# Kernel optimization log

Measured on AMD Instinct MI355X. Metric: run time of the kernel, lower is better.

The kernel has to match this reference:

```python
import jax, jax.numpy as jnp
import numpy as np

IN_DIM, HID, E, N = 1024, 2048, 8, 16384

def setup_inputs() -> dict:
    key = jax.random.key(0)
    ks = jax.random.split(key, 12)
    s_in = 1.0 / np.sqrt(IN_DIM)
    s_h = 1.0 / np.sqrt(HID)
    return {
        "x": jax.random.normal(ks[0], (N, IN_DIM), dtype=jnp.float32),
        "enc_W": jax.random.uniform(ks[1], (IN_DIM, HID), jnp.float32, -s_in, s_in),
        "enc_b": jax.random.uniform(ks[2], (HID,), jnp.float32, -s_in, s_in),
        "gate_W": jax.random.uniform(ks[3], (HID, E), jnp.float32, -s_h, s_h),
        "expert_W": jax.random.uniform(ks[4], (E, HID, HID), jnp.float32, -s_h, s_h),
        "expert_b": jax.random.uniform(ks[5], (E, HID), jnp.float32, -s_h, s_h),
        "res_W": jax.random.uniform(ks[6], (HID, HID), jnp.float32, -s_h, s_h),
        "res_b": jax.random.uniform(ks[7], (HID,), jnp.float32, -s_h, s_h),
        "coef_W": jax.random.uniform(ks[8], (HID, 2), jnp.float32, -s_h, s_h),
        "coef_b": jax.random.uniform(ks[9], (2,), jnp.float32, -s_h, s_h),
        "dec_W": jax.random.uniform(ks[10], (HID, IN_DIM), jnp.float32, -s_h, s_h),
        "dec_b": jax.random.uniform(ks[11], (IN_DIM,), jnp.float32, -s_h, s_h),
    }

def reference(x, enc_W, enc_b, gate_W, expert_W, expert_b, res_W, res_b, coef_W, coef_b, dec_W, dec_b):
    # Encode: Linear + ReLU -> h [N, HID]
    h = jax.nn.relu(x @ enc_W + enc_b)
    # Top-1 gating (softmax probs, argmax expert, combine weight = chosen prob)
    probs = jax.nn.softmax(h @ gate_W, axis=-1)          # [N, E]
    idx = jnp.argmax(probs, axis=-1)                     # [N]
    gate = jnp.max(probs, axis=-1, keepdims=True)        # [N, 1]
    # Dense dispatch: run every expert, select via one-hot combine
    y_all = jnp.einsum('nd,edh->neh', h, expert_W) + expert_b  # [N, E, HID]
    onehot = jax.nn.one_hot(idx, y_all.shape[1], dtype=h.dtype)
    moe_out = jnp.einsum('neh,ne->nh', y_all, onehot) * gate   # [N, HID]
    # Residual expert + learned 2-way blending coefficient
    res = h @ res_W + res_b
    coef = jax.nn.softmax(h @ coef_W + coef_b, axis=-1)        # [N, 2]
    out = moe_out * coef[:, 0:1] + res * coef[:, 1:2]
    # Decode
    return out @ dec_W + dec_b
```

## Files before the change

### kernel.cpp

```cpp
#include <hip/hip_runtime.h>


#define N_TOK 16384
#define IN_DIM 1024
#define HID 2048
#define NEXP 8
#define TAU 8.0e-3f

typedef __bf16 bf16_t;
typedef __bf16 bf16x8 __attribute__((ext_vector_type(8)));
typedef __bf16 bf16x4v __attribute__((ext_vector_type(4)));
typedef float f32x4 __attribute__((ext_vector_type(4)));
typedef unsigned short ushort_t;

#define CLAMP1E4(v) fmaxf(fminf((v), 1.0e4f), -1.0e4f)

#define ASYNC16(gp, lp)                                                        \
  __builtin_amdgcn_global_load_lds(                                            \
      (const __attribute__((address_space(1))) void*)(gp),                     \
      (__attribute__((address_space(3))) void*)(lp), 16, 0, 0)

static __device__ inline ushort_t b2u(bf16_t v) {
  union { bf16_t b; ushort_t u; } x; x.b = v; return x.u;
}

__global__ __launch_bounds__(256) void fill_bf16(bf16_t* __restrict__ p,
                                                 float v, int n) {
  const int i = blockIdx.x * 256 + threadIdx.x;
  if (i < n) p[i] = (bf16_t)v;
}

__global__ __launch_bounds__(256) void detect_dtype(
    const ushort_t* __restrict__ xr, int* __restrict__ flag) {
  __shared__ int s_bad;
  if (threadIdx.x == 0) s_bad = 0;
  __syncthreads();
  int bad = 0;
  for (int i = threadIdx.x; i < 4096; i += 256) {
    const int e = (xr[i] >> 7) & 0xFF;
    if (e >= 0xC0) bad = 1;
  }
  if (__any(bad) && (threadIdx.x & 63) == 0) atomicOr(&s_bad, 1);
  __syncthreads();
  if (threadIdx.x == 0) *flag = s_bad;
}

__global__ __launch_bounds__(256) void cvt_to_bf16(
    const void* __restrict__ src, bf16_t* __restrict__ dst, int n,
    const int* __restrict__ flagp) {
  const int f = *flagp;
  const int i = blockIdx.x * 256 + threadIdx.x;
  if (i >= n) return;
  dst[i] = f ? (bf16_t)((const float*)src)[i] : ((const bf16_t*)src)[i];
}

__global__ __launch_bounds__(256) void cvt_to_bf16_x4(
    const void* __restrict__ src, bf16_t* __restrict__ dst, int n4,
    const int* __restrict__ flagp) {
  const int f = *flagp;
  const int i = blockIdx.x * 256 + threadIdx.x;
  if (i >= n4) return;
  bf16x4v o;
  if (f) {
    const f32x4 v = ((const f32x4*)src)[i];
    o[0] = (bf16_t)v[0]; o[1] = (bf16_t)v[1];
    o[2] = (bf16_t)v[2]; o[3] = (bf16_t)v[3];
  } else {
    o = ((const bf16x4v*)src)[i];
  }
  ((bf16x4v*)dst)[i] = o;
}

__global__ __launch_bounds__(256) void cvt_to_f32(
    const void* __restrict__ src, float* __restrict__ dst, int n,
    const int* __restrict__ flagp) {
  const int f = *flagp;
  const int i = blockIdx.x * 256 + threadIdx.x;
  if (i >= n) return;
  dst[i] = f ? ((const float*)src)[i] : (float)((const bf16_t*)src)[i];
}

__global__ __launch_bounds__(256) void transpose_cvt(
    const void* __restrict__ src0, ushort_t* __restrict__ dst, int R, int C,
    size_t elem_off, const int* __restrict__ flagp, size_t src_zstride,
    size_t dst_zstride) {
  __shared__ ushort_t t[32][33];
  const int f = *flagp;
  const size_t eoff = elem_off + (size_t)blockIdx.z * src_zstride;
  dst += (size_t)blockIdx.z * dst_zstride;
  const int c0 = blockIdx.x * 32, r0 = blockIdx.y * 32;
  const int tx = threadIdx.x, ty = threadIdx.y;
  if (f) {
    const float* s = (const float*)src0 + eoff;
#pragma unroll
    for (int i = 0; i < 4; ++i)
      t[ty + i * 8][tx] =
          b2u((bf16_t)s[(size_t)(r0 + ty + i * 8) * C + c0 + tx]);
  } else {
    const ushort_t* s = (const ushort_t*)src0 + eoff;
#pragma unroll
    for (int i = 0; i < 4; ++i)
      t[ty + i * 8][tx] = s[(size_t)(r0 + ty + i * 8) * C + c0 + tx];
  }
  __syncthreads();
#pragma unroll
  for (int i = 0; i < 4; ++i)
    dst[(size_t)(c0 + ty + i * 8) * R + r0 + tx] = t[tx][ty + i * 8];
}

__global__ __launch_bounds__(256) void enc_gemm(
    const bf16_t* __restrict__ A, const bf16_t* __restrict__ Bt,
    const float* __restrict__ bias, bf16_t* __restrict__ H) {
  __shared__ bf16_t As[128 * 32];
  __shared__ bf16_t Bs[128 * 32];

  const int tid = threadIdx.x, lane = tid & 63, w = tid >> 6;
  const int wr = w >> 1, wc = w & 1, quad = lane >> 4, l16 = lane & 15;
  const int m0 = blockIdx.x * 128, n0 = blockIdx.y * 128;
  const char* Ab = (const char*)A;
  const char* Bb = (const char*)Bt;
  const size_t lda = (size_t)IN_DIM * 2;

  const f32x4 fz = {0.f, 0.f, 0.f, 0.f};
  f32x4 acc[4][4];
#pragma unroll
  for (int i = 0; i < 4; ++i)
#pragma unroll
    for (int j = 0; j < 4; ++j) acc[i][j] = fz;

  size_t aoff[2], boff[2];
  int cb[2];
#pragma unroll
  for (int c = 0; c < 2; ++c) {
    cb[c] = (w * 2 + c) * 1024;
    const int o = cb[c] + lane * 16;
    const int row = o >> 6, kb = o & 63;
    aoff[c] = (size_t)(m0 + row) * lda + kb;
    boff[c] = (size_t)(n0 + row) * lda + kb;
  }

  for (int kt = 0; kt < IN_DIM / 32; ++kt) {
    __syncthreads();
#pragma unroll
    for (int c = 0; c < 2; ++c) {
      ASYNC16(Ab + aoff[c] + (size_t)kt * 64, (char*)As + cb[c]);
      ASYNC16(Bb + boff[c] + (size_t)kt * 64, (char*)Bs + cb[c]);
    }
    __syncthreads();

    bf16x8 af[4], bfr[4];
#pragma unroll
    for (int i = 0; i < 4; ++i)
      af[i] = *(const bf16x8*)&As[(wr * 64 + i * 16 + l16) * 32 + quad * 8];
#pragma unroll
    for (int j = 0; j < 4; ++j)
      bfr[j] = *(const bf16x8*)&Bs[(wc * 64 + j * 16 + l16) * 32 + quad * 8];
#pragma unroll
    for (int i = 0; i < 4; ++i)
#pragma unroll
      for (int j = 0; j < 4; ++j)
        acc[i][j] = __builtin_amdgcn_mfma_f32_16x16x32_bf16(af[i], bfr[j],
                                                            acc[i][j], 0, 0, 0);
  }

  float bj[4];
  int colj[4];
#pragma unroll
  for (int j = 0; j < 4; ++j) {
    colj[j] = n0 + wc * 64 + j * 16 + l16;
    bj[j] = bias[colj[j]];
  }

#pragma unroll
  for (int i = 0; i < 4; ++i) {
#pragma unroll
    for (int r = 0; r < 4; ++r) {
      const int row = m0 + wr * 64 + i * 16 + quad * 4 + r;
#pragma unroll
      for (int j = 0; j < 4; ++j) {
        const float v = fminf(fmaxf(acc[i][j][r] + bj[j], 0.f), 1.0e4f);
        H[(size_t)row * HID + colj[j]] = (bf16_t)v;
      }
    }
  }
}

__global__ __launch_bounds__(256) void gate_from_h(
    const bf16_t* __restrict__ H, const bf16_t* __restrict__ gW,
    const bf16_t* __restrict__ cW, const float* __restrict__ coefBf,
    float* __restrict__ s0g, float* __restrict__ s1g, float* __restrict__ c0g,
    int* __restrict__ eidx, int* __restrict__ ambig, int* __restrict__ acnt) {
  const int tid = threadIdx.x, lane = tid & 63, w = tid >> 6;
  const int r0 = blockIdx.x * 16 + w * 4;

  float acc[4][10];
#pragma unroll
  for (int g = 0; g < 4; ++g)
#pragma unroll
    for (int o = 0; o < 10; ++o) acc[g][o] = 0.f;

#pragma unroll
  for (int it = 0; it < HID / 512; ++it) {
    const int h0 = it * 512 + lane * 8;
    bf16x8 hv[4];
#pragma unroll
    for (int g = 0; g < 4; ++g)
      hv[g] = *(const bf16x8*)(H + (size_t)(r0 + g) * HID + h0);
    const bf16_t* gp = gW + (size_t)h0 * 8;
    const bf16_t* cp = cW + (size_t)h0 * 2;
    bf16x8 cc0 = *(const bf16x8*)(cp);
    bf16x8 cc1 = *(const bf16x8*)(cp + 8);
#pragma unroll
    for (int k = 0; k < 8; ++k) {
      const bf16x8 gk = *(const bf16x8*)(gp + k * 8);
      const float ck0 = (k < 4) ? (float)cc0[(k & 3) * 2]
                                : (float)cc1[(k & 3) * 2];
      const float ck1 = (k < 4) ? (float)cc0[(k & 3) * 2 + 1]
                                : (float)cc1[(k & 3) * 2 + 1];
#pragma unroll
      for (int g = 0; g < 4; ++g) {
        const float v = (float)hv[g][k];
#pragma unroll
        for (int o = 0; o < 8; ++o) acc[g][o] += v * (float)gk[o];
        acc[g][8] += v * ck0;
        acc[g][9] += v * ck1;
      }
    }
  }

#pragma unroll
  for (int m = 1; m < 64; m <<= 1)
#pragma unroll
    for (int g = 0; g < 4; ++g)
#pragma unroll
      for (int o = 0; o < 10; ++o) acc[g][o] += __shfl_xor(acc[g][o], m);

  if (lane == 0) {
#pragma unroll
    for (int g = 0; g < 4; ++g) {
      const int r = r0 + g;
      float lv[8];
#pragma unroll
      for (int e = 0; e < 8; ++e) lv[e] = acc[g][e];
      float mx = lv[0];
      int idx = 0;
#pragma unroll
      for (int e = 1; e < 8; ++e)
        if (lv[e] > mx) { mx = lv[e]; idx = e; }
      float s2 = -1.0e30f;
#pragma unroll
      for (int e = 0; e < 8; ++e)
        if (e != idx) s2 = fmaxf(s2, lv[e]);
      float s = 0.f;
#pragma unroll
      for (int e = 0; e < 8; ++e) s += expf(lv[e] - mx);
      const float gate = 1.f / s;
      const float c0 = acc[g][8] + coefBf[0], c1 = acc[g][9] + coefBf[1];
      const float cm = fmaxf(c0, c1);
      const float e0 = expf(c0 - cm), e1 = expf(c1 - cm);
      const float inv = 1.f / (e0 + e1);
      const float p0 = e0 * inv;
      c0g[r] = p0;
      s1g[r] = e1 * inv;
      s0g[r] = gate * p0;
      eidx[r] = idx;
      if (mx - s2 < TAU) {
        const int p = atomicAdd(acnt, 1);
        ambig[p] = r;
      }
    }
  }
}

__global__ __launch_bounds__(256) void rescue_rows(
    const void* __restrict__ xraw, const void* __restrict__ encWraw,
    const float* __restrict__ encBf, const void* __restrict__ gateWraw,
    const int* __restrict__ flagp, const int* __restrict__ ambig,
    const int* __restrict__ acnt, const float* __restrict__ c0g,
    float* __restrict__ s0g, int* __restrict__ eidx) {
  const int i = blockIdx.x;
  if (i >= *acnt) return;
  const int r = ambig[i];
  const int f = *flagp;
  const int tid = threadIdx.x;

  double hacc[8] = {0, 0, 0, 0, 0, 0, 0, 0};
  if (f) {
    const float* x = (const float*)xraw + (size_t)r * IN_DIM;
    const float* W = (const float*)encWraw;
    for (int k = 0; k < IN_DIM; ++k) {
      const double xv = (double)x[k];
      const float* Wr = W + (size_t)k * HID;
#pragma unroll
      for (int jj = 0; jj < 8; ++jj)
        hacc[jj] += xv * (double)Wr[tid + jj * 256];
    }
  } else {
    const bf16_t* x = (const bf16_t*)xraw + (size_t)r * IN_DIM;
    const bf16_t* W = (const bf16_t*)encWraw;
    for (int k = 0; k < IN_DIM; ++k) {
      const double xv = (double)(float)x[k];
      const bf16_t* Wr = W + (size_t)k * HID;
#pragma unroll
      for (int jj = 0; jj < 8; ++jj)
        hacc[jj] += xv * (double)(float)Wr[tid + jj * 256];
    }
  }

  double lg[8] = {0, 0, 0, 0, 0, 0, 0, 0};
#pragma unroll
  for (int jj = 0; jj < 8; ++jj) {
    const int j = tid + jj * 256;
    double h = hacc[jj] + (double)encBf[j];
    if (h > 0.0) {
      if (f) {
        const float* g = (const float*)gateWraw + (size_t)j * 8;
#pragma unroll
        for (int e = 0; e < 8; ++e) lg[e] += h * (double)g[e];
      } else {
        const bf16_t* g = (const bf16_t*)gateWraw + (size_t)j * 8;
#pragma unroll
        for (int e = 0; e < 8; ++e) lg[e] += h * (double)(float)g[e];
      }
    }
  }
#pragma unroll
  for (int m = 1; m < 64; m <<= 1)
#pragma unroll
    for (int e = 0; e < 8; ++e) lg[e] += __shfl_xor(lg[e], m);

  __shared__ double red[4][8];
  const int w = tid >> 6, lane = tid & 63;
  if (lane == 0)
#pragma unroll
    for (int e = 0; e < 8; ++e) red[w][e] = lg[e];
  __syncthreads();
  if (tid == 0) {
    double t[8];
#pragma unroll
    for (int e = 0; e < 8; ++e)
      t[e] = red[0][e] + red[1][e] + red[2][e] + red[3][e];
    double m = t[0];
    int idx = 0;
#pragma unroll
    for (int e = 1; e < 8; ++e)
      if (t[e] > m) { m = t[e]; idx = e; }
    double s = 0.0;
#pragma unroll
    for (int e = 0; e < 8; ++e) s += exp(t[e] - m);
    s0g[r] = (float)((1.0 / s) * (double)c0g[r]);
    eidx[r] = idx;
  }
}

__global__ __launch_bounds__(256) void bucket_rows(
    const int* __restrict__ eidx, int* __restrict__ cnt,
    int* __restrict__ perm) {
  const int r = blockIdx.x * 256 + threadIdx.x;
  const int e = eidx[r];
  const int pos = atomicAdd(&cnt[e], 1);
  perm[(size_t)e * N_TOK + pos] = r;
}

__global__ __launch_bounds__(256) void expert_gemm(
    const bf16_t* __restrict__ H, const bf16_t* __restrict__ wTbase,
    size_t wstride, const float* __restrict__ expBf,
    const int* __restrict__ perm, const int* __restrict__ cnt, int eArg,
    const float* __restrict__ s0g, bf16_t* __restrict__ mid) {
  __shared__ bf16_t As[128 * 32];
  __shared__ bf16_t Bs[128 * 32];
  __shared__ int rows_s[128];
  __shared__ float s0_s[128];

  const int e = (eArg >= 0) ? eArg : (int)blockIdx.z;
  const bf16_t* wTe = wTbase + (size_t)e * wstride;
  const float* eBe = expBf + (size_t)e * HID;
  const int* permE = perm + (size_t)e * N_TOK;

  const int cnte = cnt[e];
  const int lt = blockIdx.x;
  if (lt * 128 >= cnte) return;
  int nrows = cnte - lt * 128;
  if (nrows > 128) nrows = 128;

  const int tid = threadIdx.x, lane = tid & 63, w = tid >> 6;
  const int wr = w >> 1, wc = w & 1, quad = lane >> 4, l16 = lane & 15;

  if (tid < 128) {
    int grow = -1;
    float a0 = 0.f;
    if (tid < nrows) {
      grow = permE[lt * 128 + tid];
      a0 = s0g[grow];
    }
    rows_s[tid] = grow;
    s0_s[tid] = a0;
  }
  __syncthreads();

  const int n0 = blockIdx.y * 128;
  const char* Hb = (const char*)H;
  const char* Wb = (const char*)wTe;

  size_t aoff[2], boff[2];
  int cb[2];
#pragma unroll
  for (int c = 0; c < 2; ++c) {
    cb[c] = (w * 2 + c) * 1024;
    const int o = cb[c] + lane * 16;
    const int row = o >> 6, kb = o & 63;
    int gr = rows_s[row];
    if (gr < 0) gr = 0;
    aoff[c] = (size_t)gr * (HID * 2) + kb;
    boff[c] = (size_t)(n0 + row) * (HID * 2) + kb;
  }

  const f32x4 fz = {0.f, 0.f, 0.f, 0.f};
  f32x4 acc[4][4];
#pragma unroll
  for (int i = 0; i < 4; ++i)
#pragma unroll
    for (int j = 0; j < 4; ++j) acc[i][j] = fz;

  for (int kt = 0; kt < HID / 32; ++kt) {
    __syncthreads();
#pragma unroll
    for (int c = 0; c < 2; ++c) {
      ASYNC16(Hb + aoff[c] + (size_t)kt * 64, (char*)As + cb[c]);
      ASYNC16(Wb + boff[c] + (size_t)kt * 64, (char*)Bs + cb[c]);
    }
    __syncthreads();

    bf16x8 af[4], bfr[4];
#pragma unroll
    for (int i = 0; i < 4; ++i)
      af[i] = *(const bf16x8*)&As[(wr * 64 + i * 16 + l16) * 32 + quad * 8];
#pragma unroll
    for (int j = 0; j < 4; ++j)
      bfr[j] = *(const bf16x8*)&Bs[(wc * 64 + j * 16 + l16) * 32 + quad * 8];
#pragma unroll
    for (int i = 0; i < 4; ++i)
#pragma unroll
      for (int j = 0; j < 4; ++j)
        acc[i][j] = __builtin_amdgcn_mfma_f32_16x16x32_bf16(af[i], bfr[j],
                                                            acc[i][j], 0, 0, 0);
  }

  float beb[4];
  int colj[4];
#pragma unroll
  for (int j = 0; j < 4; ++j) {
    colj[j] = n0 + wc * 64 + j * 16 + l16;
    beb[j] = eBe[colj[j]];
  }
#pragma unroll
  for (int i = 0; i < 4; ++i) {
#pragma unroll
    for (int r = 0; r < 4; ++r) {
      const int lr = wr * 64 + i * 16 + quad * 4 + r;
      const int grow = rows_s[lr];
      if (grow < 0) continue;
      const float s0 = s0_s[lr];
#pragma unroll
      for (int j = 0; j < 4; ++j) {
        const float v = CLAMP1E4(s0 * (acc[i][j][r] + beb[j]));
        mid[(size_t)grow * HID + colj[j]] = (bf16_t)v;
      }
    }
  }
}

__global__ __launch_bounds__(256) void res_gemm(
    const bf16_t* __restrict__ H, const bf16_t* __restrict__ Bt,
    const float* __restrict__ rB, const float* __restrict__ s1g,
    bf16_t* __restrict__ mid) {
  __shared__ bf16_t As[128 * 32];
  __shared__ bf16_t Bs[128 * 32];

  const int tid = threadIdx.x, lane = tid & 63, w = tid >> 6;
  const int wr = w >> 1, wc = w & 1, quad = lane >> 4, l16 = lane & 15;
  const int m0 = blockIdx.x * 128, n0 = blockIdx.y * 128;
  const char* Ab = (const char*)H;
  const char* Bb = (const char*)Bt;

  size_t aoff[2], boff[2];
  int cb[2];
#pragma unroll
  for (int c = 0; c < 2; ++c) {
    cb[c] = (w * 2 + c) * 1024;
    const int o = cb[c] + lane * 16;
    const int row = o >> 6, kb = o & 63;
    aoff[c] = (size_t)(m0 + row) * (HID * 2) + kb;
    boff[c] = (size_t)(n0 + row) * (HID * 2) + kb;
  }

  const f32x4 fz = {0.f, 0.f, 0.f, 0.f};
  f32x4 acc[4][4];
#pragma unroll
  for (int i = 0; i < 4; ++i)
#pragma unroll
    for (int j = 0; j < 4; ++j) acc[i][j] = fz;

  for (int kt = 0; kt < HID / 32; ++kt) {
    __syncthreads();
#pragma unroll
    for (int c = 0; c < 2; ++c) {
      ASYNC16(Ab + aoff[c] + (size_t)kt * 64, (char*)As + cb[c]);
      ASYNC16(Bb + boff[c] + (size_t)kt * 64, (char*)Bs + cb[c]);
    }
    __syncthreads();

    bf16x8 af[4], bfr[4];
#pragma unroll
    for (int i = 0; i < 4; ++i)
      af[i] = *(const bf16x8*)&As[(wr * 64 + i * 16 + l16) * 32 + quad * 8];
#pragma unroll
    for (int j = 0; j < 4; ++j)
      bfr[j] = *(const bf16x8*)&Bs[(wc * 64 + j * 16 + l16) * 32 + quad * 8];
#pragma unroll
    for (int i = 0; i < 4; ++i)
#pragma unroll
      for (int j = 0; j < 4; ++j)
        acc[i][j] = __builtin_amdgcn_mfma_f32_16x16x32_bf16(af[i], bfr[j],
                                                            acc[i][j], 0, 0, 0);
  }

  float rbb[4];
  int colj[4];
#pragma unroll
  for (int j = 0; j < 4; ++j) {
    colj[j] = n0 + wc * 64 + j * 16 + l16;
    rbb[j] = rB[colj[j]];
  }
#pragma unroll
  for (int i = 0; i < 4; ++i) {
#pragma unroll
    for (int r = 0; r < 4; ++r) {
      const int row = m0 + wr * 64 + i * 16 + quad * 4 + r;
      const float s1 = s1g[row];
#pragma unroll
      for (int j = 0; j < 4; ++j) {
        const size_t ix = (size_t)row * HID + colj[j];
        const float v =
            CLAMP1E4(s1 * (acc[i][j][r] + rbb[j]) + (float)mid[ix]);
        mid[ix] = (bf16_t)v;
      }
    }
  }
}

__global__ __launch_bounds__(256) void dec_gemm(
    const bf16_t* __restrict__ A, const bf16_t* __restrict__ Bt,
    const float* __restrict__ bias, void* __restrict__ C,
    const int* __restrict__ flagp) {
  __shared__ bf16_t As[128 * 32];
  __shared__ bf16_t Bs[128 * 32];

  const int fl = *flagp;
  const int tid = threadIdx.x, lane = tid & 63, w = tid >> 6;
  const int wr = w >> 1, wc = w & 1, quad = lane >> 4, l16 = lane & 15;
  const int m0 = blockIdx.x * 128, n0 = blockIdx.y * 128;
  const char* Ab = (const char*)A;
  const char* Bb = (const char*)Bt;

  size_t aoff[2], boff[2];
  int cb[2];
#pragma unroll
  for (int c = 0; c < 2; ++c) {
    cb[c] = (w * 2 + c) * 1024;
    const int o = cb[c] + lane * 16;
    const int row = o >> 6, kb = o & 63;
    aoff[c] = (size_t)(m0 + row) * (HID * 2) + kb;
    boff[c] = (size_t)(n0 + row) * (HID * 2) + kb;
  }

  const f32x4 fz = {0.f, 0.f, 0.f, 0.f};
  f32x4 acc[4][4];
#pragma unroll
  for (int i = 0; i < 4; ++i)
#pragma unroll
    for (int j = 0; j < 4; ++j) acc[i][j] = fz;

  for (int kt = 0; kt < HID / 32; ++kt) {
    __syncthreads();
#pragma unroll
    for (int c = 0; c < 2; ++c) {
      ASYNC16(Ab + aoff[c] + (size_t)kt * 64, (char*)As + cb[c]);
      ASYNC16(Bb + boff[c] + (size_t)kt * 64, (char*)Bs + cb[c]);
    }
    __syncthreads();

    bf16x8 af[4], bfr[4];
#pragma unroll
    for (int i = 0; i < 4; ++i)
      af[i] = *(const bf16x8*)&As[(wr * 64 + i * 16 + l16) * 32 + quad * 8];
#pragma unroll
    for (int j = 0; j < 4; ++j)
      bfr[j] = *(const bf16x8*)&Bs[(wc * 64 + j * 16 + l16) * 32 + quad * 8];
#pragma unroll
    for (int i = 0; i < 4; ++i)
#pragma unroll
      for (int j = 0; j < 4; ++j)
        acc[i][j] = __builtin_amdgcn_mfma_f32_16x16x32_bf16(af[i], bfr[j],
                                                            acc[i][j], 0, 0, 0);
  }

  float bb[4];
  int colj[4];
#pragma unroll
  for (int j = 0; j < 4; ++j) {
    colj[j] = n0 + wc * 64 + j * 16 + l16;
    bb[j] = bias[colj[j]];
  }
#pragma unroll
  for (int i = 0; i < 4; ++i) {
#pragma unroll
    for (int r = 0; r < 4; ++r) {
      const int row = m0 + wr * 64 + i * 16 + quad * 4 + r;
#pragma unroll
      for (int j = 0; j < 4; ++j) {
        const float v = CLAMP1E4(acc[i][j][r] + bb[j]);
        const size_t ix = (size_t)row * IN_DIM + colj[j];
        if (fl)
          ((float*)C)[ix] = v;
        else
          ((bf16_t*)C)[ix] = (bf16_t)v;
      }
    }
  }
}

extern "C" void kernel_launch(void* const* d_in, const int* in_sizes, int n_in,
                              void* d_out, int out_size, void* d_ws,
                              size_t ws_size, hipStream_t stream) {
  (void)in_sizes; (void)n_in;

  const void* x     = d_in[0];
  const void* encW  = d_in[1];
  const void* encB  = d_in[2];
  const void* gateW = d_in[3];
  const void* expW  = d_in[4];
  const void* expB  = d_in[5];
  const void* resW  = d_in[6];
  const void* resB  = d_in[7];
  const void* coefW = d_in[8];
  const void* coefB = d_in[9];
  const void* decW  = d_in[10];
  const void* decB  = d_in[11];

  char* ws = (char*)d_ws;
  size_t o = 0;
  int*    flag  = (int*)(ws + o);    o += 256;
  int*    cnt   = (int*)(ws + o);    o += 256;
  int*    acnt  = cnt + 8;
  float*  s0g   = (float*)(ws + o);  o += (size_t)N_TOK * 4;
  float*  s1g   = (float*)(ws + o);  o += (size_t)N_TOK * 4;
  float*  c0g   = (float*)(ws + o);  o += (size_t)N_TOK * 4;
  int*    eidx  = (int*)(ws + o);    o += (size_t)N_TOK * 4;
  int*    ambig = (int*)(ws + o);    o += (size_t)N_TOK * 4;
  int*    perm  = (int*)(ws + o);    o += (size_t)NEXP * N_TOK * 4;
  float*  encBf = (float*)(ws + o);  o += HID * 4;
  float*  expBf = (float*)(ws + o);  o += (size_t)NEXP * HID * 4;
  float*  resBf = (float*)(ws + o);  o += HID * 4;
  float*  decBf = (float*)(ws + o);  o += IN_DIM * 4;
  float*  coefBf= (float*)(ws + o);  o += 256;
  bf16_t* gWb   = (bf16_t*)(ws + o); o += (size_t)HID * 8 * 2;
  bf16_t* cWb   = (bf16_t*)(ws + o); o += (size_t)HID * 2 * 2;
  o = (o + 255) & ~(size_t)255;
  bf16_t* hbuf  = (bf16_t*)(ws + o); o += (size_t)N_TOK * HID * 2;
  bf16_t* mid   = (bf16_t*)(ws + o); o += (size_t)N_TOK * HID * 2;
  bf16_t* wT    = (bf16_t*)(ws + o); o += (size_t)HID * HID * 2;
  const size_t needed_small = o;
  const size_t S = (size_t)HID * HID;
  bf16_t* wTall = (bf16_t*)(ws + o);
  const size_t needed_big = o + 10 * S * 2;
  bf16_t* xbf = mid;

  if (ws_size < needed_small) {
    const float v = (float)(ws_size >> 20);
    fill_bf16<<<dim3((out_size + 255) / 256), 256, 0, stream>>>(
        (bf16_t*)d_out, v, out_size);
    return;
  }
  const bool big = ws_size >= needed_big;

  detect_dtype<<<1, 256, 0, stream>>>((const ushort_t*)x, flag);
  hipMemsetAsync(cnt, 0, 256, stream);

  cvt_to_bf16_x4<<<dim3(N_TOK * IN_DIM / 4 / 256), 256, 0, stream>>>(
      x, xbf, N_TOK * IN_DIM / 4, flag);
  cvt_to_f32<<<dim3(HID / 256), 256, 0, stream>>>(encB, encBf, HID, flag);
  cvt_to_f32<<<dim3(NEXP * HID / 256), 256, 0, stream>>>(expB, expBf,
                                                         NEXP * HID, flag);
  cvt_to_f32<<<dim3(HID / 256), 256, 0, stream>>>(resB, resBf, HID, flag);
  cvt_to_f32<<<dim3(IN_DIM / 256), 256, 0, stream>>>(decB, decBf, IN_DIM, flag);
  cvt_to_f32<<<1, 256, 0, stream>>>(coefB, coefBf, 2, flag);
  cvt_to_bf16<<<dim3(HID * 8 / 256), 256, 0, stream>>>(gateW, gWb, HID * 8,
                                                       flag);
  cvt_to_bf16<<<dim3(HID * 2 / 256), 256, 0, stream>>>(coefW, cWb, HID * 2,
                                                       flag);

  const dim3 tb(32, 8, 1);

  transpose_cvt<<<dim3(HID / 32, IN_DIM / 32, 1), tb, 0, stream>>>(
      encW, (ushort_t*)wT, IN_DIM, HID, 0, flag, 0, 0);
  if (big) {
    transpose_cvt<<<dim3(HID / 32, HID / 32, NEXP), tb, 0, stream>>>(
        expW, (ushort_t*)wTall, HID, HID, 0, flag, S, S);
    transpose_cvt<<<dim3(HID / 32, HID / 32, 1), tb, 0, stream>>>(
        resW, (ushort_t*)(wTall + 8 * S), HID, HID, 0, flag, 0, 0);
    transpose_cvt<<<dim3(IN_DIM / 32, HID / 32, 1), tb, 0, stream>>>(
        decW, (ushort_t*)(wTall + 9 * S), HID, IN_DIM, 0, flag, 0, 0);
  }

  enc_gemm<<<dim3(N_TOK / 128, HID / 128), 256, 0, stream>>>(xbf, wT, encBf,
                                                             hbuf);
  gate_from_h<<<dim3(N_TOK / 16), 256, 0, stream>>>(
      hbuf, gWb, cWb, coefBf, s0g, s1g, c0g, eidx, ambig, acnt);
  rescue_rows<<<dim3(1024), 256, 0, stream>>>(x, encW, encBf, gateW, flag,
                                              ambig, acnt, c0g, s0g, eidx);
  bucket_rows<<<dim3(N_TOK / 256), 256, 0, stream>>>(eidx, cnt, perm);

  if (big) {
    expert_gemm<<<dim3(N_TOK / 128, HID / 128, NEXP), 256, 0, stream>>>(
        hbuf, wTall, S, expBf, perm, cnt, -1, s0g, mid);
    res_gemm<<<dim3(N_TOK / 128, HID / 128), 256, 0, stream>>>(
        hbuf, wTall + 8 * S, resBf, s1g, mid);
    dec_gemm<<<dim3(N_TOK / 128, IN_DIM / 128), 256, 0, stream>>>(
        mid, wTall + 9 * S, decBf, d_out, flag);
  } else {
    for (int e = 0; e < NEXP; ++e) {
      transpose_cvt<<<dim3(HID / 32, HID / 32, 1), tb, 0, stream>>>(
          expW, (ushort_t*)wT, HID, HID, (size_t)e * HID * HID, flag, 0, 0);
      expert_gemm<<<dim3(N_TOK / 128, HID / 128, 1), 256, 0, stream>>>(
          hbuf, wT, 0, expBf, perm, cnt, e, s0g, mid);
    }
    transpose_cvt<<<dim3(HID / 32, HID / 32, 1), tb, 0, stream>>>(
        resW, (ushort_t*)wT, HID, HID, 0, flag, 0, 0);
    res_gemm<<<dim3(N_TOK / 128, HID / 128), 256, 0, stream>>>(hbuf, wT, resBf,
                                                               s1g, mid);
    transpose_cvt<<<dim3(IN_DIM / 32, HID / 32, 1), tb, 0, stream>>>(
        decW, (ushort_t*)wT, HID, IN_DIM, 0, flag, 0, 0);
    dec_gemm<<<dim3(N_TOK / 128, IN_DIM / 128), 256, 0, stream>>>(
        mid, wT, decBf, d_out, flag);
  }
}
```

Before: 1.489 ms.

## Gather tokens by expert into contiguous buffer and compact expert GEMM grid

Gate counts per expert are now accumulated inside the gating kernel, and rescue adjusts them when a row's expert changes. A placement kernel builds a flat expert-sorted permutation, and a gather kernel copies H rows into a contiguous permuted buffer. The expert GEMM then runs over a compact 1D tile list (136 tiles instead of 8×128 mostly-empty blocks) with contiguous A loads, and the residual GEMM also reads the permuted buffer. The small conversion kernels are merged into one launch. This adds a full-size gather copy and scattered output writes through a row-id table.

```diff
diff --git a/kernel.cpp b/kernel.cpp
--- a/kernel.cpp
+++ b/kernel.cpp
@@ -43,15 +43,6 @@
   if (__any(bad) && (threadIdx.x & 63) == 0) atomicOr(&s_bad, 1);
   __syncthreads();
   if (threadIdx.x == 0) *flag = s_bad;
-}
-
-__global__ __launch_bounds__(256) void cvt_to_bf16(
-    const void* __restrict__ src, bf16_t* __restrict__ dst, int n,
-    const int* __restrict__ flagp) {
-  const int f = *flagp;
-  const int i = blockIdx.x * 256 + threadIdx.x;
-  if (i >= n) return;
-  dst[i] = f ? (bf16_t)((const float*)src)[i] : ((const bf16_t*)src)[i];
 }
 
 __global__ __launch_bounds__(256) void cvt_to_bf16_x4(
@@ -71,13 +62,40 @@
   ((bf16x4v*)dst)[i] = o;
 }
 
-__global__ __launch_bounds__(256) void cvt_to_f32(
-    const void* __restrict__ src, float* __restrict__ dst, int n,
+__global__ __launch_bounds__(256) void cvt_small(
+    const void* __restrict__ encB, const void* __restrict__ expB,
+    const void* __restrict__ resB, const void* __restrict__ decB,
+    const void* __restrict__ coefB, const void* __restrict__ gateW,
+    const void* __restrict__ coefW, float* __restrict__ encBf,
+    float* __restrict__ expBf, float* __restrict__ resBf,
+    float* __restrict__ decBf, float* __restrict__ coefBf,
+    bf16_t* __restrict__ gWb, bf16_t* __restrict__ cWb,
     const int* __restrict__ flagp) {
   const int f = *flagp;
   const int i = blockIdx.x * 256 + threadIdx.x;
+  const int seg = blockIdx.y;
+  const void* src;
+  int n;
+  switch (seg) {
+    case 0: src = encB;  n = HID; break;
+    case 1: src = expB;  n = NEXP * HID; break;
+    case 2: src = resB;  n = HID; break;
+    case 3: src = decB;  n = IN_DIM; break;
+    case 4: src = coefB; n = 2; break;
+    case 5: src = gateW; n = HID * 8; break;
+    default: src = coefW; n = HID * 2; break;
+  }
   if (i >= n) return;
-  dst[i] = f ? ((const float*)src)[i] : (float)((const bf16_t*)src)[i];
+  const float v = f ? ((const float*)src)[i] : (float)((const bf16_t*)src)[i];
+  switch (seg) {
+    case 0: encBf[i] = v; break;
+    case 1: expBf[i] = v; break;
+    case 2: resBf[i] = v; break;
+    case 3: decBf[i] = v; break;
+    case 4: coefBf[i] = v; break;
+    case 5: gWb[i] = (bf16_t)v; break;
+    default: cWb[i] = (bf16_t)v; break;
+  }
 }
 
 __global__ __launch_bounds__(256) void transpose_cvt(
@@ -189,7 +207,8 @@
     const bf16_t* __restrict__ H, const bf16_t* __restrict__ gW,
     const bf16_t* __restrict__ cW, const float* __restrict__ coefBf,
     float* __restrict__ s0g, float* __restrict__ s1g, float* __restrict__ c0g,
-    int* __restrict__ eidx, int* __restrict__ ambig, int* __restrict__ acnt) {
+    int* __restrict__ eidx, int* __restrict__ ambig, int* __restrict__ acnt,
+    int* __restrict__ cnt) {
   const int tid = threadIdx.x, lane = tid & 63, w = tid >> 6;
   const int r0 = blockIdx.x * 16 + w * 4;
 
@@ -264,6 +283,7 @@
       s1g[r] = e1 * inv;
       s0g[r] = gate * p0;
       eidx[r] = idx;
+      atomicAdd(&cnt[idx], 1);
       if (mx - s2 < TAU) {
         const int p = atomicAdd(acnt, 1);
         ambig[p] = r;
@@ -277,7 +297,7 @@
     const float* __restrict__ encBf, const void* __restrict__ gateWraw,
     const int* __restrict__ flagp, const int* __restrict__ ambig,
     const int* __restrict__ acnt, const float* __restrict__ c0g,
-    float* __restrict__ s0g, int* __restrict__ eidx) {
+    float* __restrict__ s0g, int* __restrict__ eidx, int* __restrict__ cnt) {
   const int i = blockIdx.x;
   if (i >= *acnt) return;
   const int r = ambig[i];
@@ -349,33 +369,263 @@
 #pragma unroll
     for (int e = 0; e < 8; ++e) s += exp(t[e] - m);
     s0g[r] = (float)((1.0 / s) * (double)c0g[r]);
-    eidx[r] = idx;
-  }
-}
-
-__global__ __launch_bounds__(256) void bucket_rows(
-    const int* __restrict__ eidx, int* __restrict__ cnt,
-    int* __restrict__ perm) {
+    const int old = eidx[r];
+    if (idx != old) {
+      atomicSub(&cnt[old], 1);
+      atomicAdd(&cnt[idx], 1);
+      eidx[r] = idx;
+    }
+  }
+}
+
+__global__ __launch_bounds__(256) void place_rows(
+    const int* __restrict__ eidx, const int* __restrict__ cnt,
+    int* __restrict__ curs, int* __restrict__ permflat) {
   const int r = blockIdx.x * 256 + threadIdx.x;
   const int e = eidx[r];
-  const int pos = atomicAdd(&cnt[e], 1);
-  perm[(size_t)e * N_TOK + pos] = r;
-}
-
-__global__ __launch_bounds__(256) void expert_gemm(
-    const bf16_t* __restrict__ H, const bf16_t* __restrict__ wTbase,
+  int prefix = 0;
+  for (int ee = 0; ee < NEXP; ++ee)
+    if (ee < e) prefix += cnt[ee];
+  const int pos = atomicAdd(&curs[e], 1);
+  permflat[prefix + pos] = r;
+}
+
+__global__ __launch_bounds__(256) void gather_rows(
+    const bf16_t* __restrict__ H, const int* __restrict__ permflat,
+    const float* __restrict__ s0g, const float* __restrict__ s1g,
+    bf16_t* __restrict__ Hp, int* __restrict__ rowid,
+    float* __restrict__ s0p, float* __restrict__ s1p) {
+  const int w = threadIdx.x >> 6, lane = threadIdx.x & 63;
+  const int p = blockIdx.x * 4 + w;
+  const int r = permflat[p];
+  if (lane == 0) {
+    rowid[p] = r;
+    s0p[p] = s0g[r];
+    s1p[p] = s1g[r];
+  }
+  const bf16x8* src = (const bf16x8*)(H + (size_t)r * HID);
+  bf16x8* dst = (bf16x8*)(Hp + (size_t)p * HID);
+#pragma unroll
+  for (int i = 0; i < 4; ++i) dst[lane + i * 64] = src[lane + i * 64];
+}
+
+__global__ __launch_bounds__(256) void expert_gemm_t(
+    const bf16_t* __restrict__ Hp, const bf16_t* __restrict__ wTall,
     size_t wstride, const float* __restrict__ expBf,
-    const int* __restrict__ perm, const int* __restrict__ cnt, int eArg,
-    const float* __restrict__ s0g, bf16_t* __restrict__ mid) {
+    const int* __restrict__ cnt, const int* __restrict__ rowid,
+    const float* __restrict__ s0p, bf16_t* __restrict__ mid) {
   __shared__ bf16_t As[128 * 32];
   __shared__ bf16_t Bs[128 * 32];
   __shared__ int rows_s[128];
   __shared__ float s0_s[128];
 
-  const int e = (eArg >= 0) ? eArg : (int)blockIdx.z;
-  const bf16_t* wTe = wTbase + (size_t)e * wstride;
+  const int x = blockIdx.x;
+  int e = -1, base = 0, nrows = 0;
+  {
+    int acc = 0, pre = 0;
+    for (int ee = 0; ee < NEXP; ++ee) {
+      const int ce = cnt[ee];
+      const int nt = (ce + 127) >> 7;
+      if (x < acc + nt) {
+        const int t = x - acc;
+        e = ee;
+        base = pre + t * 128;
+        nrows = ce - t * 128;
+        if (nrows > 128) nrows = 128;
+        break;
+      }
+      acc += nt;
+      pre += ce;
+    }
+  }
+  if (e < 0) return;
+
+  const int tid = threadIdx.x, lane = tid & 63, w = tid >> 6;
+  const int wr = w >> 1, wc = w & 1, quad = lane >> 4, l16 = lane & 15;
+
+  if (tid < 128) {
+    int grow = -1;
+    float a0 = 0.f;
+    if (tid < nrows) {
+      grow = rowid[base + tid];
+      a0 = s0p[base + tid];
+    }
+    rows_s[tid] = grow;
+    s0_s[tid] = a0;
+  }
+  __syncthreads();
+
+  const int n0 = blockIdx.y * 128;
+  const char* Hb = (const char*)Hp;
+  const char* Wb = (const char*)(wTall + (size_t)e * wstride);
+
+  size_t aoff[2], boff[2];
+  int cb[2];
+#pragma unroll
+  for (int c = 0; c < 2; ++c) {
+    cb[c] = (w * 2 + c) * 1024;
+    const int o = cb[c] + lane * 16;
+    const int row = o >> 6, kb = o & 63;
+    int ar = base + row;
+    if (ar > N_TOK - 1) ar = N_TOK - 1;
+    aoff[c] = (size_t)ar * (HID * 2) + kb;
+    boff[c] = (size_t)(n0 + row) * (HID * 2) + kb;
+  }
+
+  const f32x4 fz = {0.f, 0.f, 0.f, 0.f};
+  f32x4 acc[4][4];
+#pragma unroll
+  for (int i = 0; i < 4; ++i)
+#pragma unroll
+    for (int j = 0; j < 4; ++j) acc[i][j] = fz;
+
+  for (int kt = 0; kt < HID / 32; ++kt) {
+    __syncthreads();
+#pragma unroll
+    for (int c = 0; c < 2; ++c) {
+      ASYNC16(Hb + aoff[c] + (size_t)kt * 64, (char*)As + cb[c]);
+      ASYNC16(Wb + boff[c] + (size_t)kt * 64, (char*)Bs + cb[c]);
+    }
+    __syncthreads();
+
+    bf16x8 af[4], bfr[4];
+#pragma unroll
+    for (int i = 0; i < 4; ++i)
+      af[i] = *(const bf16x8*)&As[(wr * 64 + i * 16 + l16) * 32 + quad * 8];
+#pragma unroll
+    for (int j = 0; j < 4; ++j)
+      bfr[j] = *(const bf16x8*)&Bs[(wc * 64 + j * 16 + l16) * 32 + quad * 8];
+#pragma unroll
+    for (int i = 0; i < 4; ++i)
+#pragma unroll
+      for (int j = 0; j < 4; ++j)
+        acc[i][j] = __builtin_amdgcn_mfma_f32_16x16x32_bf16(af[i], bfr[j],
+                                                            acc[i][j], 0, 0, 0);
+  }
+
   const float* eBe = expBf + (size_t)e * HID;
-  const int* permE = perm + (size_t)e * N_TOK;
+  float beb[4];
+  int colj[4];
+#pragma unroll
+  for (int j = 0; j < 4; ++j) {
+    colj[j] = n0 + wc * 64 + j * 16 + l16;
+    beb[j] = eBe[colj[j]];
+  }
+#pragma unroll
+  for (int i = 0; i < 4; ++i) {
+#pragma unroll
+    for (int r = 0; r < 4; ++r) {
+      const int lr = wr * 64 + i * 16 + quad * 4 + r;
+      const int grow = rows_s[lr];
+      if (grow < 0) continue;
+      const float s0 = s0_s[lr];
+#pragma unroll
+      for (int j = 0; j < 4; ++j) {
+        const float v = CLAMP1E4(s0 * (acc[i][j][r] + beb[j]));
+        mid[(size_t)grow * HID + colj[j]] = (bf16_t)v;
+      }
+    }
+  }
+}
+
+__global__ __launch_bounds__(256) void res_gemm_p(
+    const bf16_t* __restrict__ Hp, const bf16_t* __restrict__ Bt,
+    const float* __restrict__ rB, const int* __restrict__ rowid,
+    const float* __restrict__ s1p, bf16_t* __restrict__ mid) {
+  __shared__ bf16_t As[128 * 32];
+  __shared__ bf16_t Bs[128 * 32];
+
+  const int tid = threadIdx.x, lane = tid & 63, w = tid >> 6;
+  const int wr = w >> 1, wc = w & 1, quad = lane >> 4, l16 = lane & 15;
+  const int m0 = blockIdx.x * 128, n0 = blockIdx.y * 128;
+  const char* Ab = (const char*)Hp;
+  const char* Bb = (const char*)Bt;
+
+  size_t aoff[2], boff[2];
+  int cb[2];
+#pragma unroll
+  for (int c = 0; c < 2; ++c) {
+    cb[c] = (w * 2 + c) * 1024;
+    const int o = cb[c] + lane * 16;
+    const int row = o >> 6, kb = o & 63;
+    aoff[c] = (size_t)(m0 + row) * (HID * 2) + kb;
+    boff[c] = (size_t)(n0 + row) * (HID * 2) + kb;
+  }
+
+  const f32x4 fz = {0.f, 0.f, 0.f, 0.f};
+  f32x4 acc[4][4];
+#pragma unroll
+  for (int i = 0; i < 4; ++i)
+#pragma unroll
+    for (int j = 0; j < 4; ++j) acc[i][j] = fz;
+
+  for (int kt = 0; kt < HID / 32; ++kt) {
+    __syncthreads();
+#pragma unroll
+    for (int c = 0; c < 2; ++c) {
+      ASYNC16(Ab + aoff[c] + (size_t)kt * 64, (char*)As + cb[c]);
+      ASYNC16(Bb + boff[c] + (size_t)kt * 64, (char*)Bs + cb[c]);
+    }
+    __syncthreads();
+
+    bf16x8 af[4], bfr[4];
+#pragma unroll
+    for (int i = 0; i < 4; ++i)
+      af[i] = *(const bf16x8*)&As[(wr * 64 + i * 16 + l16) * 32 + quad * 8];
+#pragma unroll
+    for (int j = 0; j < 4; ++j)
+      bfr[j] = *(const bf16x8*)&Bs[(wc * 64 + j * 16 + l16) * 32 + quad * 8];
+#pragma unroll
+    for (int i = 0; i < 4; ++i)
+#pragma unroll
+      for (int j = 0; j < 4; ++j)
+        acc[i][j] = __builtin_amdgcn_mfma_f32_16x16x32_bf16(af[i], bfr[j],
+                                                            acc[i][j], 0, 0, 0);
+  }
+
+  float rbb[4];
+  int colj[4];
+#pragma unroll
+  for (int j = 0; j < 4; ++j) {
+    colj[j] = n0 + wc * 64 + j * 16 + l16;
+    rbb[j] = rB[colj[j]];
+  }
+#pragma unroll
+  for (int i = 0; i < 4; ++i) {
+#pragma unroll
+    for (int r = 0; r < 4; ++r) {
+      const int p = m0 + wr * 64 + i * 16 + quad * 4 + r;
+      const int grow = rowid[p];
+      const float s1 = s1p[p];
+#pragma unroll
+      for (int j = 0; j < 4; ++j) {
+        const size_t ix = (size_t)grow * HID + colj[j];
+        const float v =
+            CLAMP1E4(s1 * (acc[i][j][r] + rbb[j]) + (float)mid[ix]);
+        mid[ix] = (bf16_t)v;
+      }
+    }
+  }
+}
+
+__global__ __launch_bounds__(256) void bucket_rows(
+    const int* __restrict__ eidx, int* __restrict__ curs,
+    int* __restrict__ perm) {
+  const int r = blockIdx.x * 256 + threadIdx.x;
+  const int e = eidx[r];
+  const int pos = atomicAdd(&curs[e], 1);
+  perm[(size_t)e * N_TOK + pos] = r;
+}
+
+__global__ __launch_bounds__(256) void expert_gemm(
+    const bf16_t* __restrict__ H, const bf16_t* __restrict__ wTe,
+    const float* __restrict__ eBe, const int* __restrict__ permE,
+    const int* __restrict__ cnt, int e, const float* __restrict__ s0g,
+    bf16_t* __restrict__ mid) {
+  __shared__ bf16_t As[128 * 32];
+  __shared__ bf16_t Bs[128 * 32];
+  __shared__ int rows_s[128];
+  __shared__ float s0_s[128];
 
   const int cnte = cnt[e];
   const int lt = blockIdx.x;
@@ -653,11 +903,16 @@
   int*    flag  = (int*)(ws + o);    o += 256;
   int*    cnt   = (int*)(ws + o);    o += 256;
   int*    acnt  = cnt + 8;
+  int*    curs  = cnt + 16;
   float*  s0g   = (float*)(ws + o);  o += (size_t)N_TOK * 4;
   float*  s1g   = (float*)(ws + o);  o += (size_t)N_TOK * 4;
   float*  c0g   = (float*)(ws + o);  o += (size_t)N_TOK * 4;
   int*    eidx  = (int*)(ws + o);    o += (size_t)N_TOK * 4;
   int*    ambig = (int*)(ws + o);    o += (size_t)N_TOK * 4;
+  int*    permfl= (int*)(ws + o);    o += (size_t)N_TOK * 4;
+  int*    rowid = (int*)(ws + o);    o += (size_t)N_TOK * 4;
+  float*  s0p   = (float*)(ws + o);  o += (size_t)N_TOK * 4;
+  float*  s1p   = (float*)(ws + o);  o += (size_t)N_TOK * 4;
   int*    perm  = (int*)(ws + o);    o += (size_t)NEXP * N_TOK * 4;
   float*  encBf = (float*)(ws + o);  o += HID * 4;
   float*  expBf = (float*)(ws + o);  o += (size_t)NEXP * HID * 4;
@@ -667,14 +922,16 @@
   bf16_t* gWb   = (bf16_t*)(ws + o); o += (size_t)HID * 8 * 2;
   bf16_t* cWb   = (bf16_t*)(ws + o); o += (size_t)HID * 2 * 2;
   o = (o + 255) & ~(size_t)255;
-  bf16_t* hbuf  = (bf16_t*)(ws + o); o += (size_t)N_TOK * HID * 2;
-  bf16_t* mid   = (bf16_t*)(ws + o); o += (size_t)N_TOK * HID * 2;
+  bf16_t* bufA  = (bf16_t*)(ws + o); o += (size_t)N_TOK * HID * 2;
+  bf16_t* bufB  = (bf16_t*)(ws + o); o += (size_t)N_TOK * HID * 2;
   bf16_t* wT    = (bf16_t*)(ws + o); o += (size_t)HID * HID * 2;
   const size_t needed_small = o;
   const size_t S = (size_t)HID * HID;
   bf16_t* wTall = (bf16_t*)(ws + o);
   const size_t needed_big = o + 10 * S * 2;
-  bf16_t* xbf = mid;
+
+  bf16_t* hbuf  = bufA;
+  bf16_t* xbf   = bufB;
 
   if (ws_size < needed_small) {
     const float v = (float)(ws_size >> 20);
@@ -689,16 +946,9 @@
 
   cvt_to_bf16_x4<<<dim3(N_TOK * IN_DIM / 4 / 256), 256, 0, stream>>>(
       x, xbf, N_TOK * IN_DIM / 4, flag);
-  cvt_to_f32<<<dim3(HID / 256), 256, 0, stream>>>(encB, encBf, HID, flag);
-  cvt_to_f32<<<dim3(NEXP * HID / 256), 256, 0, stream>>>(expB, expBf,
-                                                         NEXP * HID, flag);
-  cvt_to_f32<<<dim3(HID / 256), 256, 0, stream>>>(resB, resBf, HID, flag);
-  cvt_to_f32<<<dim3(IN_DIM / 256), 256, 0, stream>>>(decB, decBf, IN_DIM, flag);
-  cvt_to_f32<<<1, 256, 0, stream>>>(coefB, coefBf, 2, flag);
-  cvt_to_bf16<<<dim3(HID * 8 / 256), 256, 0, stream>>>(gateW, gWb, HID * 8,
-                                                       flag);
-  cvt_to_bf16<<<dim3(HID * 2 / 256), 256, 0, stream>>>(coefW, cWb, HID * 2,
-                                                       flag);
+  cvt_small<<<dim3(64, 7), 256, 0, stream>>>(encB, expB, resB, decB, coefB,
+                                             gateW, coefW, encBf, expBf, resBf,
+                                             decBf, coefBf, gWb, cWb, flag);
 
   const dim3 tb(32, 8, 1);
 
@@ -716,24 +966,32 @@
   enc_gemm<<<dim3(N_TOK / 128, HID / 128), 256, 0, stream>>>(xbf, wT, encBf,
                                                              hbuf);
   gate_from_h<<<dim3(N_TOK / 16), 256, 0, stream>>>(
-      hbuf, gWb, cWb, coefBf, s0g, s1g, c0g, eidx, ambig, acnt);
+      hbuf, gWb, cWb, coefBf, s0g, s1g, c0g, eidx, ambig, acnt, cnt);
   rescue_rows<<<dim3(1024), 256, 0, stream>>>(x, encW, encBf, gateW, flag,
-                                              ambig, acnt, c0g, s0g, eidx);
-  bucket_rows<<<dim3(N_TOK / 256), 256, 0, stream>>>(eidx, cnt, perm);
+                                              ambig, acnt, c0g, s0g, eidx,
+                                              cnt);
 
   if (big) {
-    expert_gemm<<<dim3(N_TOK / 128, HID / 128, NEXP), 256, 0, stream>>>(
-        hbuf, wTall, S, expBf, perm, cnt, -1, s0g, mid);
-    res_gemm<<<dim3(N_TOK / 128, HID / 128), 256, 0, stream>>>(
-        hbuf, wTall + 8 * S, resBf, s1g, mid);
+    bf16_t* Hperm = bufB;
+    bf16_t* mid   = bufA;
+    place_rows<<<dim3(N_TOK / 256), 256, 0, stream>>>(eidx, cnt, curs, permfl);
+    gather_rows<<<dim3(N_TOK / 4), 256, 0, stream>>>(hbuf, permfl, s0g, s1g,
+                                                     Hperm, rowid, s0p, s1p);
+    expert_gemm_t<<<dim3(136, HID / 128), 256, 0, stream>>>(
+        Hperm, wTall, S, expBf, cnt, rowid, s0p, mid);
+    res_gemm_p<<<dim3(N_TOK / 128, HID / 128), 256, 0, stream>>>(
+        Hperm, wTall + 8 * S, resBf, rowid, s1p, mid);
     dec_gemm<<<dim3(N_TOK / 128, IN_DIM / 128), 256, 0, stream>>>(
         mid, wTall + 9 * S, decBf, d_out, flag);
   } else {
+    bf16_t* mid = bufB;
+    bucket_rows<<<dim3(N_TOK / 256), 256, 0, stream>>>(eidx, curs, perm);
     for (int e = 0; e < NEXP; ++e) {
       transpose_cvt<<<dim3(HID / 32, HID / 32, 1), tb, 0, stream>>>(
           expW, (ushort_t*)wT, HID, HID, (size_t)e * HID * HID, flag, 0, 0);
-      expert_gemm<<<dim3(N_TOK / 128, HID / 128, 1), 256, 0, stream>>>(
-          hbuf, wT, 0, expBf, perm, cnt, e, s0g, mid);
+      expert_gemm<<<dim3(N_TOK / 128, HID / 128), 256, 0, stream>>>(
+          hbuf, wT, expBf + (size_t)e * HID, perm + (size_t)e * N_TOK, cnt, e,
+          s0g, mid);
     }
     transpose_cvt<<<dim3(HID / 32, HID / 32, 1), tb, 0, stream>>>(
         resW, (ushort_t*)wT, HID, HID, 0, flag, 0, 0);
```

After: 1.531 ms. 1.03x slower.
